# Kernel optimization log

Hardware: AMD Instinct MI355X
Metric: run time of the kernel (lower is better)

Reference implementation:

```python
import jax, jax.numpy as jnp
import numpy as np

E = 8        # numExperts
D = 1024     # d_model
F = 4096     # expert hidden = 4*d_model
T = 8192     # total tokens (sum of expertFrequency)


def setup_inputs() -> dict:
    key = jax.random.key(0)
    k0, k1, k2, k3, k4 = jax.random.split(key, 5)
    expertOrderedInput = jax.random.normal(k0, (T, D), dtype=jnp.float32)
    # Static equal split so the split sizes are jit-compatible.
    expertFrequency = jnp.full((E,), T // E, dtype=jnp.int64)
    s1 = 1.0 / np.sqrt(D)
    s2 = 1.0 / np.sqrt(F)
    w1 = jax.random.normal(k1, (E, D, F), dtype=jnp.float32) * s1
    b1 = jnp.zeros((E, F), dtype=jnp.float32)
    w2 = jax.random.normal(k2, (E, F, D), dtype=jnp.float32) * s2
    b2 = jnp.zeros((E, D), dtype=jnp.float32)
    return {"expertOrderedInput": expertOrderedInput,
            "expertFrequency": expertFrequency,
            "w1": w1, "b1": b1, "w2": w2, "b2": b2}


def reference(expertOrderedInput, expertFrequency, w1, b1, w2, b2):
    # expertOrderedInput: [T, D], tokens pre-sorted by expert.
    # expertFrequency is equal per expert (T/E each), so the
    # split-loop-cat in the torch module is exactly a grouped GEMM.
    e = w1.shape[0]
    t = expertOrderedInput.shape[0]
    x = expertOrderedInput.reshape(e, t // e, -1)            # [E, T/E, D]
    h = jax.nn.gelu(jnp.einsum('etd,edf->etf', x, w1) + b1[:, None, :])
    y = jnp.einsum('etf,efd->etd', h, w2) + b2[:, None, :]   # [E, T/E, D]
    return y.reshape(t, -1)                                   # cat along dim 0
```

## Files before the change

### kernel.cpp

```cpp
#include <hip/hip_runtime.h>

#define E_ 8
#define D_ 1024
#define F_ 4096
#define T_ 8192

typedef unsigned short u16;
typedef short bf16x8 __attribute__((ext_vector_type(8)));
typedef float f32x4 __attribute__((ext_vector_type(4)));
typedef unsigned short u16x8 __attribute__((ext_vector_type(8)));
typedef unsigned short u16x2 __attribute__((ext_vector_type(2)));

__device__ __forceinline__ u16 f2bf(float f) {
    unsigned u = __builtin_bit_cast(unsigned, f);
    u += 0x7fffu + ((u >> 16) & 1u);
    return (u16)(u >> 16);
}

__device__ __forceinline__ float gelu_fast(float x) {
    const float a = -2.885390082f * 0.7978845608028654f;
    const float b = a * 0.044715f;
    float u = x * x;
    float p = x * __builtin_fmaf(b, u, a);
    float e = exp2f(p);
    return x * __builtin_amdgcn_rcpf(1.0f + e);
}

__device__ __forceinline__ void async16(const void* g, void* l) {
    __builtin_amdgcn_global_load_lds(
        (const __attribute__((address_space(1))) unsigned int*)g,
        (__attribute__((address_space(3))) unsigned int*)l, 16, 0, 0);
}

__global__ void cvt_x(const float* __restrict__ in, u16* __restrict__ out) {
    int i = blockIdx.x * 256 + threadIdx.x;
    const float4* in4 = (const float4*)in;
    float4 a = in4[2 * i], b = in4[2 * i + 1];
    u16x8 o;
    o[0] = f2bf(a.x); o[1] = f2bf(a.y); o[2] = f2bf(a.z); o[3] = f2bf(a.w);
    o[4] = f2bf(b.x); o[5] = f2bf(b.y); o[6] = f2bf(b.z); o[7] = f2bf(b.w);
    *(u16x8*)(out + (size_t)i * 8) = o;
}

__global__ __launch_bounds__(256) void transpose_cvt(
    const float* __restrict__ src, u16* __restrict__ dst, int R, int C) {
    __shared__ float tile[32][129];
    int e = blockIdx.z;
    src += (size_t)e * R * C;
    dst += (size_t)e * R * C;
    int c0 = blockIdx.x * 32, r0 = blockIdx.y * 128;
    int tid = threadIdx.x;
    int lc = tid & 31, lr0 = tid >> 5;
#pragma unroll
    for (int i = 0; i < 16; ++i) {
        int r = lr0 + i * 8;
        tile[lc][r] = src[(size_t)(r0 + r) * C + c0 + lc];
    }
    __syncthreads();
    int sc = tid >> 6, sr = (tid & 63) * 2;
#pragma unroll
    for (int i = 0; i < 8; ++i) {
        int c = sc + i * 4;
        u16x2 v;
        v[0] = f2bf(tile[c][sr]);
        v[1] = f2bf(tile[c][sr + 1]);
        *(u16x2*)(dst + (size_t)(c0 + c) * R + r0 + sr) = v;
    }
}

template <int BN, int EPI, int NM, int NN>
__global__ __launch_bounds__(512, 2) void gemm4p(
    const u16* __restrict__ A,
    const u16* __restrict__ Bt,
    const float* __restrict__ bias,
    void* __restrict__ Cv,
    int Mpe, int N, int K) {
    constexpr int BM  = 256;
    constexpr int LA  = 2;
    constexpr int LB  = BN / 128;
    constexpr int MFR = 4;
    constexpr int NFR = BN / 2 / 16;
    constexpr int NH  = NFR / 2;
    constexpr int AELEM = 4 * BM * 32;
    constexpr int VMP = 2 * LA + LB;
    constexpr int VMT = LA + LB;
    constexpr int VPR = 2 * (LA + LB);
    __shared__ u16 lds[AELEM + 4 * BN * 32];

    const int tid = threadIdx.x;
    const int w = tid >> 6, lane = tid & 63;
    const int lr = lane & 15, lg = lane >> 4;
    const int wm = w >> 1, wn = w & 1;

    constexpr int NWG = E_ * NM * NN;
    constexpr int PER = NWG / 8;
    const int bid = blockIdx.x;
    const int logical = (bid & 7) * PER + (bid >> 3);
    const int e   = logical / (NM * NN);
    const int rem = logical % (NM * NN);
    const int bn  = rem / NM;
    const int bm  = rem % NM;

    A    += (size_t)e * Mpe * K;
    Bt   += (size_t)e * N * K;
    bias += (size_t)e * N;
    const int n0 = bn * BN;
    const int m0 = bm * BM;
    const int NT = K >> 6;

    const char* gA[LA];
    const char* gB[LB];
    {
        int kch = (lane & 3) ^ ((lane >> 3) & 3);
#pragma unroll
        for (int i = 0; i < LA; ++i) {
            int row = i * 128 + w * 16 + (lane >> 2);
            gA[i] = (const char*)(A + (size_t)(m0 + row) * K + kch * 8);
        }
#pragma unroll
        for (int i = 0; i < LB; ++i) {
            int row = i * 128 + w * 16 + (lane >> 2);
            gB[i] = (const char*)(Bt + (size_t)(n0 + row) * K + kch * 8);
        }
    }
    char* ldsc = (char*)lds;

    auto stageA = [&](int t, int h) {
        size_t goff = (size_t)t * 128 + (size_t)h * 64;
        unsigned dst = (unsigned)((((t & 1) * 2 + h) * (BM * 64)) + w * 1024);
#pragma unroll
        for (int i = 0; i < LA; ++i)
            async16(gA[i] + goff, ldsc + dst + i * 8192);
    };
    auto stageB = [&](int t, int h) {
        size_t goff = (size_t)t * 128 + (size_t)h * 64;
        unsigned dst = (unsigned)(AELEM * 2 + (((t & 1) * 2 + h) * (BN * 64)) + w * 1024);
#pragma unroll
        for (int i = 0; i < LB; ++i)
            async16(gB[i] + goff, ldsc + dst + i * 8192);
    };

    f32x4 acc[MFR][NFR];
    const f32x4 zero = {0.f, 0.f, 0.f, 0.f};
#pragma unroll
    for (int i = 0; i < MFR; ++i)
#pragma unroll
        for (int j = 0; j < NFR; ++j) acc[i][j] = zero;

    const u16* SBbase = lds + AELEM;
    const int arow = wm * 64 + lr;
    const int nbase = wn * (BN / 2) + lr;
    const int axor = (lg ^ ((arow >> 1) & 3)) * 8;
    const int bxor = (lg ^ ((nbase >> 1) & 3)) * 8;

    bf16x8 a_cur[MFR], a_nxt[MFR], bA[NH], bB[NH];

    stageA(0, 0); stageB(0, 0); stageA(0, 1); stageB(0, 1);
    stageA(1, 0); stageB(1, 0);
    asm volatile("s_waitcnt vmcnt(%0)" :: "i"(VPR) : "memory");
    __builtin_amdgcn_s_barrier();
    __builtin_amdgcn_sched_barrier(0);
    {
        const u16* SA0 = lds;
        const u16* SB0 = SBbase;
#pragma unroll
        for (int i = 0; i < MFR; ++i)
            a_cur[i] = *(const bf16x8*)(SA0 + (arow + i * 16) * 32 + axor);
#pragma unroll
        for (int j = 0; j < NH; ++j)
            bA[j] = *(const bf16x8*)(SB0 + (nbase + j * 16) * 32 + bxor);
    }
    asm volatile("s_waitcnt lgkmcnt(0)" ::: "memory");
    __builtin_amdgcn_sched_barrier(0);

#define MFMA_BLK(AARR, BARR, J0)                                              \
    __builtin_amdgcn_s_setprio(1);                                            \
    _Pragma("unroll")                                                         \
    for (int i = 0; i < MFR; ++i) {                                           \
        _Pragma("unroll")                                                     \
        for (int j = 0; j < NH; ++j)                                          \
            acc[i][(J0) + j] = __builtin_amdgcn_mfma_f32_16x16x32_bf16(       \
                AARR[i], BARR[j], acc[i][(J0) + j], 0, 0, 0);                 \
    }                                                                         \
    __builtin_amdgcn_s_setprio(0);

#define PH_END()                                           \
    __builtin_amdgcn_sched_barrier(0);                     \
    asm volatile("s_waitcnt lgkmcnt(0)" ::: "memory");     \
    __builtin_amdgcn_s_barrier();                          \
    __builtin_amdgcn_sched_barrier(0);

#pragma unroll 2
    for (int c = 0; c < NT; ++c) {
        const int bb = c & 1;
        const u16* SA0 = lds    + (bb * 2 + 0) * (BM * 32);
        const u16* SA1 = lds    + (bb * 2 + 1) * (BM * 32);
        const u16* SB0 = SBbase + (bb * 2 + 0) * (BN * 32);
        const u16* SB1 = SBbase + (bb * 2 + 1) * (BN * 32);
        const u16* SA0n = lds    + (((c + 1) & 1) * 2) * (BM * 32);
        const u16* SB0n = SBbase + (((c + 1) & 1) * 2) * (BN * 32);
        const bool stg1 = (c + 1 < NT);
        const bool stg2 = (c + 2 < NT);

#pragma unroll
        for (int j = 0; j < NH; ++j)
            bB[j] = *(const bf16x8*)(SB0 + (nbase + (NH + j) * 16) * 32 + bxor);
        if (stg1) stageA(c + 1, 1);
        __builtin_amdgcn_sched_barrier(0);
        MFMA_BLK(a_cur, bA, 0);
        __builtin_amdgcn_sched_barrier(0);
        asm volatile("s_waitcnt lgkmcnt(0)" ::: "memory");
        if (c == NT - 1) asm volatile("s_waitcnt vmcnt(0)" ::: "memory");
        else             asm volatile("s_waitcnt vmcnt(%0)" :: "i"(VMP) : "memory");
        __builtin_amdgcn_s_barrier();
        __builtin_amdgcn_sched_barrier(0);

#pragma unroll
        for (int i = 0; i < MFR; ++i)
            a_nxt[i] = *(const bf16x8*)(SA1 + (arow + i * 16) * 32 + axor);
#pragma unroll
        for (int j = 0; j < NH; ++j)
            bA[j] = *(const bf16x8*)(SB1 + (nbase + j * 16) * 32 + bxor);
        if (stg1) stageB(c + 1, 1);
        __builtin_amdgcn_sched_barrier(0);
        MFMA_BLK(a_cur, bB, NH);
        PH_END();

#pragma unroll
        for (int j = 0; j < NH; ++j)
            bB[j] = *(const bf16x8*)(SB1 + (nbase + (NH + j) * 16) * 32 + bxor);
        if (stg2) stageA(c + 2, 0);
        __builtin_amdgcn_sched_barrier(0);
        MFMA_BLK(a_nxt, bA, 0);
        __builtin_amdgcn_sched_barrier(0);
        asm volatile("s_waitcnt lgkmcnt(0)" ::: "memory");
        if (c == NT - 1)      asm volatile("s_waitcnt vmcnt(0)" ::: "memory");
        else if (c == NT - 2) asm volatile("s_waitcnt vmcnt(%0)" :: "i"(VMT) : "memory");
        else                  asm volatile("s_waitcnt vmcnt(%0)" :: "i"(VMP) : "memory");
        __builtin_amdgcn_s_barrier();
        __builtin_amdgcn_sched_barrier(0);

        if (c + 1 < NT) {
#pragma unroll
            for (int i = 0; i < MFR; ++i)
                a_cur[i] = *(const bf16x8*)(SA0n + (arow + i * 16) * 32 + axor);
#pragma unroll
            for (int j = 0; j < NH; ++j)
                bA[j] = *(const bf16x8*)(SB0n + (nbase + j * 16) * 32 + bxor);
        }
        if (stg2) stageB(c + 2, 0);
        __builtin_amdgcn_sched_barrier(0);
        MFMA_BLK(a_nxt, bB, NH);
        PH_END();
    }
#undef MFMA_BLK
#undef PH_END

    const int mb = m0 + wm * 64, nb = n0 + wn * (BN / 2);
    if constexpr (EPI == 1) {
        u16* C = (u16*)Cv + (size_t)e * Mpe * N;
#pragma unroll
        for (int i = 0; i < MFR; ++i) {
#pragma unroll
            for (int j = 0; j < NFR; ++j) {
                int col = nb + j * 16 + lr;
                float bv = bias[col];
                int row = mb + i * 16 + lg * 4;
#pragma unroll
                for (int t = 0; t < 4; ++t) {
                    float v = acc[i][j][t] + bv;
                    C[(size_t)(row + t) * N + col] = f2bf(gelu_fast(v));
                }
            }
        }
    } else {
        float* C = (float*)Cv + (size_t)e * Mpe * N;
#pragma unroll
        for (int i = 0; i < MFR; ++i) {
#pragma unroll
            for (int j = 0; j < NFR; ++j) {
                int col = nb + j * 16 + lr;
                float bv = bias[col];
                int row = mb + i * 16 + lg * 4;
#pragma unroll
                for (int t = 0; t < 4; ++t)
                    C[(size_t)(row + t) * N + col] = acc[i][j][t] + bv;
            }
        }
    }
}

extern "C" void kernel_launch(void* const* d_in, const int* in_sizes, int n_in,
                              void* d_out, int out_size, void* d_ws, size_t ws_size,
                              hipStream_t stream) {
    const float* X  = (const float*)d_in[0];
    const float* w1 = (const float*)d_in[2];
    const float* b1 = (const float*)d_in[3];
    const float* w2 = (const float*)d_in[4];
    const float* b2 = (const float*)d_in[5];
    float* out = (float*)d_out;

    const size_t XBF_B = (size_t)T_ * D_ * 2;
    const size_t WT_B  = (size_t)E_ * F_ * D_ * 2;
    const size_t H_B   = (size_t)T_ * F_ * 2;
    if (ws_size < XBF_B + WT_B + H_B) return;

    char* ws = (char*)d_ws;
    u16* Xbf = (u16*)ws;
    u16* Wt  = (u16*)(ws + XBF_B);
    u16* H   = (u16*)(ws + XBF_B + WT_B);

    cvt_x<<<dim3((T_ * D_) / 8 / 256), dim3(256), 0, stream>>>(X, Xbf);
    transpose_cvt<<<dim3(F_ / 32, D_ / 128, E_), dim3(256), 0, stream>>>(w1, Wt, D_, F_);
    gemm4p<256, 1, 4, 16><<<dim3(512), dim3(512), 0, stream>>>(
        Xbf, Wt, b1, H, T_ / E_, F_, D_);
    transpose_cvt<<<dim3(D_ / 32, F_ / 128, E_), dim3(256), 0, stream>>>(w2, Wt, F_, D_);
    gemm4p<128, 0, 4, 8><<<dim3(256), dim3(512), 0, stream>>>(
        H, Wt, b2, out, T_ / E_, D_, F_);
}
```

Measured before the change: 248.4 us.

## Restructure GEMM main loop from four to two barrier phases per iteration

Rewrites the software-pipelined MFMA loop so each iteration uses two barrier-separated phases instead of four. Each phase issues all LDS reads for the next sub-tile plus both A and B global prefetches up front, then uses a partial lgkmcnt wait between the two MFMA sub-blocks. The goal is to cut workgroup barrier and waitcnt stalls and give MFMAs more overlap with LDS and global loads. In exchange the kernel holds an extra B fragment array in registers, which raises register pressure and risks spilling under the 512x2 launch bounds.

```diff
diff --git a/kernel.cpp b/kernel.cpp
--- a/kernel.cpp
+++ b/kernel.cpp
@@ -69,7 +69,7 @@
 }
 
 template <int BN, int EPI, int NM, int NN>
-__global__ __launch_bounds__(512, 2) void gemm4p(
+__global__ __launch_bounds__(512, 2) void gemm2p(
     const u16* __restrict__ A,
     const u16* __restrict__ Bt,
     const float* __restrict__ bias,
@@ -79,12 +79,11 @@
     constexpr int LA  = 2;
     constexpr int LB  = BN / 128;
     constexpr int MFR = 4;
-    constexpr int NFR = BN / 2 / 16;
+    constexpr int NFR = BN / 32;
     constexpr int NH  = NFR / 2;
     constexpr int AELEM = 4 * BM * 32;
-    constexpr int VMP = 2 * LA + LB;
-    constexpr int VMT = LA + LB;
-    constexpr int VPR = 2 * (LA + LB);
+    constexpr int VMS = LA + LB;
+    constexpr int LGP = NH + 4;
     __shared__ u16 lds[AELEM + 4 * BN * 32];
 
     const int tid = threadIdx.x;
@@ -147,33 +146,30 @@
 #pragma unroll
         for (int j = 0; j < NFR; ++j) acc[i][j] = zero;
 
-    const u16* SBbase = lds + AELEM;
+    const u16* SBb = lds + AELEM;
     const int arow = wm * 64 + lr;
     const int nbase = wn * (BN / 2) + lr;
     const int axor = (lg ^ ((arow >> 1) & 3)) * 8;
     const int bxor = (lg ^ ((nbase >> 1) & 3)) * 8;
 
-    bf16x8 a_cur[MFR], a_nxt[MFR], bA[NH], bB[NH];
+    bf16x8 aC[MFR], aN[MFR], bloA[NH], bloB[NH], bhi[NH];
 
     stageA(0, 0); stageB(0, 0); stageA(0, 1); stageB(0, 1);
-    stageA(1, 0); stageB(1, 0);
-    asm volatile("s_waitcnt vmcnt(%0)" :: "i"(VPR) : "memory");
+    if (NT > 1) { stageA(1, 0); stageB(1, 0); }
+    if (NT > 1) asm volatile("s_waitcnt vmcnt(%0)" :: "i"(VMS) : "memory");
+    else        asm volatile("s_waitcnt vmcnt(0)" ::: "memory");
     __builtin_amdgcn_s_barrier();
     __builtin_amdgcn_sched_barrier(0);
-    {
-        const u16* SA0 = lds;
-        const u16* SB0 = SBbase;
-#pragma unroll
-        for (int i = 0; i < MFR; ++i)
-            a_cur[i] = *(const bf16x8*)(SA0 + (arow + i * 16) * 32 + axor);
-#pragma unroll
-        for (int j = 0; j < NH; ++j)
-            bA[j] = *(const bf16x8*)(SB0 + (nbase + j * 16) * 32 + bxor);
-    }
+#pragma unroll
+    for (int i = 0; i < MFR; ++i)
+        aC[i] = *(const bf16x8*)(lds + (arow + i * 16) * 32 + axor);
+#pragma unroll
+    for (int j = 0; j < NH; ++j)
+        bloA[j] = *(const bf16x8*)(SBb + (nbase + j * 16) * 32 + bxor);
     asm volatile("s_waitcnt lgkmcnt(0)" ::: "memory");
     __builtin_amdgcn_sched_barrier(0);
 
-#define MFMA_BLK(AARR, BARR, J0)                                              \
+#define MFMA_SUB(AARR, BARR, J0)                                              \
     __builtin_amdgcn_s_setprio(1);                                            \
     _Pragma("unroll")                                                         \
     for (int i = 0; i < MFR; ++i) {                                           \
@@ -184,77 +180,70 @@
     }                                                                         \
     __builtin_amdgcn_s_setprio(0);
 
-#define PH_END()                                           \
-    __builtin_amdgcn_sched_barrier(0);                     \
-    asm volatile("s_waitcnt lgkmcnt(0)" ::: "memory");     \
-    __builtin_amdgcn_s_barrier();                          \
-    __builtin_amdgcn_sched_barrier(0);
-
 #pragma unroll 2
     for (int c = 0; c < NT; ++c) {
         const int bb = c & 1;
-        const u16* SA0 = lds    + (bb * 2 + 0) * (BM * 32);
-        const u16* SA1 = lds    + (bb * 2 + 1) * (BM * 32);
-        const u16* SB0 = SBbase + (bb * 2 + 0) * (BN * 32);
-        const u16* SB1 = SBbase + (bb * 2 + 1) * (BN * 32);
-        const u16* SA0n = lds    + (((c + 1) & 1) * 2) * (BM * 32);
-        const u16* SB0n = SBbase + (((c + 1) & 1) * 2) * (BN * 32);
+        const u16* SA0 = lds + (bb * 2 + 0) * (BM * 32);
+        const u16* SA1 = lds + (bb * 2 + 1) * (BM * 32);
+        const u16* SB0 = SBb + (bb * 2 + 0) * (BN * 32);
+        const u16* SB1 = SBb + (bb * 2 + 1) * (BN * 32);
+        const u16* SA0n = lds + ((bb ^ 1) * 2) * (BM * 32);
+        const u16* SB0n = SBb + ((bb ^ 1) * 2) * (BN * 32);
         const bool stg1 = (c + 1 < NT);
         const bool stg2 = (c + 2 < NT);
 
 #pragma unroll
         for (int j = 0; j < NH; ++j)
-            bB[j] = *(const bf16x8*)(SB0 + (nbase + (NH + j) * 16) * 32 + bxor);
-        if (stg1) stageA(c + 1, 1);
-        __builtin_amdgcn_sched_barrier(0);
-        MFMA_BLK(a_cur, bA, 0);
+            bhi[j] = *(const bf16x8*)(SB0 + (nbase + (NH + j) * 16) * 32 + bxor);
+        __builtin_amdgcn_sched_barrier(0);
+#pragma unroll
+        for (int i = 0; i < MFR; ++i)
+            aN[i] = *(const bf16x8*)(SA1 + (arow + i * 16) * 32 + axor);
+#pragma unroll
+        for (int j = 0; j < NH; ++j)
+            bloB[j] = *(const bf16x8*)(SB1 + (nbase + j * 16) * 32 + bxor);
+        if (stg1) { stageA(c + 1, 1); stageB(c + 1, 1); }
+        __builtin_amdgcn_sched_barrier(0);
+        MFMA_SUB(aC, bloA, 0);
+        __builtin_amdgcn_sched_barrier(0);
+        asm volatile("s_waitcnt lgkmcnt(%0)" :: "i"(LGP) : "memory");
+        __builtin_amdgcn_sched_barrier(0);
+        MFMA_SUB(aC, bhi, NH);
         __builtin_amdgcn_sched_barrier(0);
         asm volatile("s_waitcnt lgkmcnt(0)" ::: "memory");
-        if (c == NT - 1) asm volatile("s_waitcnt vmcnt(0)" ::: "memory");
-        else             asm volatile("s_waitcnt vmcnt(%0)" :: "i"(VMP) : "memory");
+        if (stg1) asm volatile("s_waitcnt vmcnt(%0)" :: "i"(VMS) : "memory");
+        else      asm volatile("s_waitcnt vmcnt(0)" ::: "memory");
         __builtin_amdgcn_s_barrier();
         __builtin_amdgcn_sched_barrier(0);
 
 #pragma unroll
-        for (int i = 0; i < MFR; ++i)
-            a_nxt[i] = *(const bf16x8*)(SA1 + (arow + i * 16) * 32 + axor);
-#pragma unroll
         for (int j = 0; j < NH; ++j)
-            bA[j] = *(const bf16x8*)(SB1 + (nbase + j * 16) * 32 + bxor);
-        if (stg1) stageB(c + 1, 1);
-        __builtin_amdgcn_sched_barrier(0);
-        MFMA_BLK(a_cur, bB, NH);
-        PH_END();
-
-#pragma unroll
-        for (int j = 0; j < NH; ++j)
-            bB[j] = *(const bf16x8*)(SB1 + (nbase + (NH + j) * 16) * 32 + bxor);
-        if (stg2) stageA(c + 2, 0);
-        __builtin_amdgcn_sched_barrier(0);
-        MFMA_BLK(a_nxt, bA, 0);
+            bhi[j] = *(const bf16x8*)(SB1 + (nbase + (NH + j) * 16) * 32 + bxor);
+        __builtin_amdgcn_sched_barrier(0);
+        if (stg1) {
+#pragma unroll
+            for (int i = 0; i < MFR; ++i)
+                aC[i] = *(const bf16x8*)(SA0n + (arow + i * 16) * 32 + axor);
+#pragma unroll
+            for (int j = 0; j < NH; ++j)
+                bloA[j] = *(const bf16x8*)(SB0n + (nbase + j * 16) * 32 + bxor);
+            stageA(c + 2, 0) , stageB(c + 2, 0);
+        }
+        __builtin_amdgcn_sched_barrier(0);
+        MFMA_SUB(aN, bloB, 0);
+        __builtin_amdgcn_sched_barrier(0);
+        if (stg1) asm volatile("s_waitcnt lgkmcnt(%0)" :: "i"(LGP) : "memory");
+        else      asm volatile("s_waitcnt lgkmcnt(0)" ::: "memory");
+        __builtin_amdgcn_sched_barrier(0);
+        MFMA_SUB(aN, bhi, NH);
         __builtin_amdgcn_sched_barrier(0);
         asm volatile("s_waitcnt lgkmcnt(0)" ::: "memory");
-        if (c == NT - 1)      asm volatile("s_waitcnt vmcnt(0)" ::: "memory");
-        else if (c == NT - 2) asm volatile("s_waitcnt vmcnt(%0)" :: "i"(VMT) : "memory");
-        else                  asm volatile("s_waitcnt vmcnt(%0)" :: "i"(VMP) : "memory");
+        if (stg2) asm volatile("s_waitcnt vmcnt(%0)" :: "i"(VMS) : "memory");
+        else      asm volatile("s_waitcnt vmcnt(0)" ::: "memory");
         __builtin_amdgcn_s_barrier();
         __builtin_amdgcn_sched_barrier(0);
-
-        if (c + 1 < NT) {
-#pragma unroll
-            for (int i = 0; i < MFR; ++i)
-                a_cur[i] = *(const bf16x8*)(SA0n + (arow + i * 16) * 32 + axor);
-#pragma unroll
-            for (int j = 0; j < NH; ++j)
-                bA[j] = *(const bf16x8*)(SB0n + (nbase + j * 16) * 32 + bxor);
-        }
-        if (stg2) stageB(c + 2, 0);
-        __builtin_amdgcn_sched_barrier(0);
-        MFMA_BLK(a_nxt, bB, NH);
-        PH_END();
-    }
-#undef MFMA_BLK
-#undef PH_END
+    }
+#undef MFMA_SUB
 
     const int mb = m0 + wm * 64, nb = n0 + wn * (BN / 2);
     if constexpr (EPI == 1) {
@@ -312,9 +301,9 @@
 
     cvt_x<<<dim3((T_ * D_) / 8 / 256), dim3(256), 0, stream>>>(X, Xbf);
     transpose_cvt<<<dim3(F_ / 32, D_ / 128, E_), dim3(256), 0, stream>>>(w1, Wt, D_, F_);
-    gemm4p<256, 1, 4, 16><<<dim3(512), dim3(512), 0, stream>>>(
+    gemm2p<256, 1, 4, 16><<<dim3(512), dim3(512), 0, stream>>>(
         Xbf, Wt, b1, H, T_ / E_, F_, D_);
     transpose_cvt<<<dim3(D_ / 32, F_ / 128, E_), dim3(256), 0, stream>>>(w2, Wt, F_, D_);
-    gemm4p<128, 0, 4, 8><<<dim3(256), dim3(512), 0, stream>>>(
+    gemm2p<128, 0, 4, 8><<<dim3(256), dim3(512), 0, stream>>>(
         H, Wt, b2, out, T_ / E_, D_, F_);
 }
```

Measured after the change: 242.3 us. -2.5%, faster.
